# Performance work log

Hardware: AMD Instinct MI355X
Metric: run time of the kernel (lower is better)

Reference implementation:

```python
import jax, jax.numpy as jnp
import numpy as np

# ---- static frequency grid from init kwargs ----
POS_FREQS = 31
W_MIN, W_MAX = 0.1, 1.0
PATCH = 16

def _build_grid():
    g = (W_MAX / W_MIN) ** (1.0 / (POS_FREQS - 1))
    pos_w = (W_MIN * g ** np.arange(POS_FREQS)).astype(np.float32)
    Wx = np.concatenate([-pos_w[::-1], [0.0], pos_w]).astype(np.float32)  # len 63
    Wy = np.concatenate([[0.0], pos_w]).astype(np.float32)               # len 32
    pad_h = (PATCH - len(Wx) % PATCH) % PATCH  # 1 -> H=64
    pad_w = (PATCH - len(Wy) % PATCH) % PATCH  # 0 -> W=32
    U, V = np.meshgrid(Wx, Wy, indexing='ij')
    U = np.pad(U, ((0, pad_h), (0, pad_w))).astype(np.float32)
    V = np.pad(V, ((0, pad_h), (0, pad_w))).astype(np.float32)
    pad_mask = np.ones_like(U)
    if pad_h > 0:
        pad_mask[-pad_h:, :] = 0.0
    if pad_w > 0:
        pad_mask[:, -pad_w:] = 0.0
    return U, V, pad_mask

_U, _V, _PADMASK = _build_grid()
H, W = _U.shape


def _cft_triangles(tris):
    """Closed-form CFT of each triangle over the HxW frequency grid.
    tris: [T,3,2] float32 -> [T,H,W] complex64."""
    pi = np.float32(np.pi)
    U = jnp.asarray(_U)[None]  # [1,H,W]
    V = jnp.asarray(_V)[None]
    xq = tris[:, 0, 0][:, None, None]; yq = tris[:, 0, 1][:, None, None]
    xr = tris[:, 1, 0][:, None, None]; yr = tris[:, 1, 1][:, None, None]
    xs = tris[:, 2, 0][:, None, None]; ys = tris[:, 2, 1][:, None, None]
    det = xq * (yr - ys) + xr * (ys - yq) + xs * (yq - yr)
    area = jnp.abs(0.5 * det)  # [T,1,1]
    U_ = U * (xr - xq) + V * (yr - yq)  # [T,H,W]
    V_ = U * (xs - xr) + V * (ys - yr)
    phase_shift = jnp.exp(-2j * pi * (U * xq + V * yq))
    zero_mask = (U_ == 0) & (V_ == 0)
    diag_mask = (U_ + V_ == 0) & ~zero_mask
    u_mask = (U_ == 0) & ~zero_mask
    v_mask = (V_ == 0) & ~zero_mask
    normal_mask = ~(diag_mask | zero_mask | u_mask | v_mask)
    four_pi2 = np.float32(4.0) * pi * pi

    def inv_safe(den, m):
        # masked reciprocal with safe denominator (keeps grads finite)
        return jnp.where(m, 1.0, 0.0) / jnp.where(m, den, 1.0)

    part1 = (inv_safe(four_pi2 * U_ * V_ * (U_ + V_), normal_mask)
             - inv_safe(four_pi2 * U_ * U_, diag_mask)
             - inv_safe(four_pi2 * V_ * V_, u_mask)
             + inv_safe(four_pi2 * U_ * U_, v_mask))
    base_u = jnp.exp(-2j * pi * U_)
    base_v = jnp.exp(-2j * pi * V_)
    base_uv = jnp.exp(-2j * pi * (U_ + V_))
    j2pi = 2j * pi
    part2 = (jnp.where(normal_mask, -U_ * base_uv + (U_ + V_) * base_u - V_, 0.0)
             + jnp.where(diag_mask, base_u + j2pi * U_ - 1.0, 0.0)
             + jnp.where(u_mask, base_v + j2pi * V_ - 1.0, 0.0)
             + jnp.where(v_mask, (j2pi * U_ + 1.0) * base_u - 1.0, 0.0))
    FT = 2.0 * area * part1 * part2 * phase_shift
    FT = jnp.where(zero_mask, area.astype(jnp.complex64), FT)
    return FT * jnp.asarray(_PADMASK)[None]


def _forward(batch_triangles, lengths):
    B, maxN = batch_triangles.shape[:2]
    FT = _cft_triangles(batch_triangles.reshape(B * maxN, 3, 2))
    FT = FT.reshape(B, maxN, H, W)
    valid = (jnp.arange(maxN)[None, :] < lengths[:, None]).astype(jnp.float32)
    FT_total = jnp.sum(FT * valid[:, :, None, None], axis=1)  # segment-sum by polygon
    re, im = FT_total.real, FT_total.imag
    m2 = re * re + im * im
    is0 = m2 == 0
    mag = jnp.where(is0, 0.0, jnp.sqrt(jnp.where(is0, 1.0, m2)))
    phase = jnp.arctan2(im, jnp.where(is0, 1.0, re))  # angle(0)=0 like torch
    mag = jnp.log1p(mag)
    return mag[:, None], phase[:, None]  # [B,1,H,W] each


def setup_inputs() -> dict:
    key = jax.random.key(0)
    k1, k2 = jax.random.split(key)
    batch_triangles = jax.random.normal(k1, (64, 128, 3, 2), dtype=jnp.float32)
    lengths = jax.random.randint(k2, (64,), 0, 128, dtype=jnp.int32)
    return {"batch_triangles": batch_triangles, "lengths": lengths}


def reference(batch_triangles, lengths):
    return _forward(batch_triangles, lengths)
```

## Files before the change

kernel.cpp:

```cpp
#include <hip/hip_runtime.h>
#include <cmath>

#define BB     64
#define MAXN   128
#define HH     64
#define WW     32
#define NFREQ  (HH*WW)
#define BLK    256
#define NWAVE  4
#define PGRPS  (NFREQ/64)

__device__ __constant__ float c_posw[31] = {
    0.10000000000f, 0.10797751623f, 0.11659144012f, 0.12589254118f,
    0.13593563909f, 0.14677992676f, 0.15848931925f, 0.17113283042f,
    0.18478497970f, 0.19952623150f, 0.21544346900f, 0.23263050672f,
    0.25118864315f, 0.27122725793f, 0.29286445646f, 0.31622776602f,
    0.34145488738f, 0.36869450645f, 0.39810717055f, 0.42986623483f,
    0.46415888336f, 0.50118723363f, 0.54116952655f, 0.58434141336f,
    0.63095734448f, 0.68129206906f, 0.73564225446f, 0.79432823472f,
    0.85769589859f, 0.92611872813f, 1.00000000000f
};

__device__ __forceinline__ void sincos_2pi(float x, float* s, float* c) {
    float r = __builtin_amdgcn_fractf(x);
    *s = __builtin_amdgcn_sinf(r);
    *c = __builtin_amdgcn_cosf(r);
}

__device__ __forceinline__ void eval_tri(
    float U, float V, float4 A4, float4 B4, float& accR, float& accI,
    float TWOPI, float FOUR_PI2)
{
    const float xq = A4.x,  yq = A4.y,  e1x = A4.z, e1y = A4.w;
    const float e2x = B4.x, e2y = B4.y, area = B4.z;

    const float U_ = __fadd_rn(__fmul_rn(U, e1x), __fmul_rn(V, e1y));
    const float V_ = __fadd_rn(__fmul_rn(U, e2x), __fmul_rn(V, e2y));
    const float S  = __fadd_rn(U_, V_);

    const bool uz   = (U_ == 0.0f);
    const bool vz   = (V_ == 0.0f);
    const bool sz   = (S  == 0.0f);
    const bool zero = uz && vz;
    const bool diag = sz && !zero;
    const bool u_m  = uz && !zero;
    const bool v_m  = vz && !zero;
    const bool nrm  = !(uz || vz || sz);

    const float t_q = U * xq + V * yq;
    const float t_r = t_q + U_;
    const float t_s = t_r + V_;

    float s_q, c_q, s_r, c_r, s_s, c_s;
    sincos_2pi(t_q, &s_q, &c_q);
    sincos_2pi(t_r, &s_r, &c_r);
    sincos_2pi(t_s, &s_s, &c_s);

    const float twU = TWOPI * U_;
    const float twV = TWOPI * V_;

    const float Ac = nrm ? -U_ : (u_m ? 1.0f : 0.0f);
    const float Bc = nrm ?  S  : ((diag || v_m) ? 1.0f : 0.0f);
    const float Cc = nrm ? -V_ : -1.0f;
    const float Dc = v_m  ? twU : 0.0f;
    const float Ec = diag ? twU : (u_m ? twV : 0.0f);

    const float d1  = u_m ? V_ : U_;
    const float den = nrm ? (U_ * V_) * S : d1 * d1;
    const float p1  = __builtin_amdgcn_rcpf(FOUR_PI2 * den);
    const float sgn = (diag || u_m) ? -2.0f : 2.0f;
    const float k   = zero ? 0.0f : sgn * area * p1;

    const float re =  Ac * c_s + Bc * c_r + Cc * c_q + Dc * s_r + Ec * s_q;
    const float im = -(Ac * s_s + Bc * s_r + Cc * s_q) + Dc * c_r + Ec * c_q;

    accR = fmaf(k, re, accR) + (zero ? area : 0.0f);
    accI = fmaf(k, im, accI);
}

__global__ __launch_bounds__(BLK) void poly_cft_fused(
    const float* __restrict__ tris,
    const int*   __restrict__ lengths,
    float*       __restrict__ out)
{
    __shared__ float2 s_red[NWAVE][64];

    const int pg   = blockIdx.x;
    const int b    = blockIdx.y;
    const int lane = threadIdx.x & 63;
    const int wv   = threadIdx.x >> 6;
    const int p    = (pg << 6) | lane;
    const int h    = p >> 5;
    const int w    = p & 31;

    float U;
    if (h < 31)       U = -c_posw[30 - h];
    else if (h == 31) U = 0.0f;
    else if (h < 63)  U = c_posw[h - 32];
    else              U = 0.0f;
    const float V = (w == 0) ? 0.0f : c_posw[w - 1];

    const float PI_F     = 3.14159274101257324f;
    const float TWOPI    = 6.28318548202514648f;
    const float FOUR_PI2 = (4.0f * PI_F) * PI_F;

    const int N = lengths[b];
    const float* __restrict__ tb = tris + (size_t)b * MAXN * 6;

    float accR = 0.0f, accI = 0.0f;

    int n = wv;
    float xq = 0.0f, yq = 0.0f, xr = 0.0f, yr = 0.0f, xs = 0.0f, ys = 0.0f;
    if (n < N) {
        const int nn = __builtin_amdgcn_readfirstlane(n);
        const float* t = tb + nn * 6;
        xq = t[0]; yq = t[1]; xr = t[2]; yr = t[3]; xs = t[4]; ys = t[5];
    }
    while (n < N) {
        const int n2 = n + NWAVE;
        float x2q = 0.0f, y2q = 0.0f, x2r = 0.0f, y2r = 0.0f, x2s = 0.0f, y2s = 0.0f;
        if (n2 < N) {
            const int nn2 = __builtin_amdgcn_readfirstlane(n2);
            const float* t2 = tb + nn2 * 6;
            x2q = t2[0]; y2q = t2[1]; x2r = t2[2]; y2r = t2[3]; x2s = t2[4]; y2s = t2[5];
        }

        const float det  = xq * (yr - ys) + xr * (ys - yq) + xs * (yq - yr);
        const float area = fabsf(0.5f * det);
        const float4 A4 = make_float4(xq, yq, xr - xq, yr - yq);
        const float4 B4 = make_float4(xs - xr, ys - yr, area, 0.0f);
        eval_tri(U, V, A4, B4, accR, accI, TWOPI, FOUR_PI2);

        n = n2;
        xq = x2q; yq = y2q; xr = x2r; yr = y2r; xs = x2s; ys = y2s;
    }

    s_red[wv][lane] = make_float2(accR, accI);
    __syncthreads();

    if (wv == 0) {
        float R = 0.0f, I = 0.0f;
#pragma unroll
        for (int k = 0; k < NWAVE; ++k) {
            const float2 v = s_red[k][lane];
            R += v.x;
            I += v.y;
        }
        R += 0.0f;
        I += 0.0f;

        if (h == 63) { R = 0.0f; I = 0.0f; }

        const float m2 = __fadd_rn(__fmul_rn(R, R), __fmul_rn(I, I));
        float mag, ph;
        if (m2 == 0.0f) {
            mag = 0.0f;
            ph  = atan2f(I, 1.0f);
        } else {
            mag = log1pf(sqrtf(m2));
            ph  = atan2f(I, R);
        }

        const int o = b * NFREQ + p;
        out[o]              = mag;
        out[BB * NFREQ + o] = ph;
    }
}

extern "C" void kernel_launch(void* const* d_in, const int* in_sizes, int n_in,
                              void* d_out, int out_size, void* d_ws, size_t ws_size,
                              hipStream_t stream) {
    const float* tris    = (const float*)d_in[0];
    const int*   lengths = (const int*)d_in[1];
    float*       out     = (float*)d_out;

    poly_cft_fused<<<dim3(PGRPS, BB), dim3(BLK), 0, stream>>>(tris, lengths, out);
}
```

Before: 80.94 us.

## Stage triangle setup in LDS and add wave-uniform fast path for generic frequencies

Each block now precomputes per-triangle edge vectors and doubled area once into shared memory, instead of every wave reloading vertices from global memory and recomputing the determinant per iteration. The inner loop uses a ballot to take a compact branch when no lane hits a degenerate case (U_, V_ or their sum equal to zero). That branch drops the mask/select logic and uses a simplified coefficient formula. This adds a block-wide barrier and LDS traffic, and the fast path must match the general formula numerically.

```diff
diff --git a/kernel.cpp b/kernel.cpp
--- a/kernel.cpp
+++ b/kernel.cpp
@@ -27,62 +27,13 @@
     *c = __builtin_amdgcn_cosf(r);
 }
 
-__device__ __forceinline__ void eval_tri(
-    float U, float V, float4 A4, float4 B4, float& accR, float& accI,
-    float TWOPI, float FOUR_PI2)
-{
-    const float xq = A4.x,  yq = A4.y,  e1x = A4.z, e1y = A4.w;
-    const float e2x = B4.x, e2y = B4.y, area = B4.z;
-
-    const float U_ = __fadd_rn(__fmul_rn(U, e1x), __fmul_rn(V, e1y));
-    const float V_ = __fadd_rn(__fmul_rn(U, e2x), __fmul_rn(V, e2y));
-    const float S  = __fadd_rn(U_, V_);
-
-    const bool uz   = (U_ == 0.0f);
-    const bool vz   = (V_ == 0.0f);
-    const bool sz   = (S  == 0.0f);
-    const bool zero = uz && vz;
-    const bool diag = sz && !zero;
-    const bool u_m  = uz && !zero;
-    const bool v_m  = vz && !zero;
-    const bool nrm  = !(uz || vz || sz);
-
-    const float t_q = U * xq + V * yq;
-    const float t_r = t_q + U_;
-    const float t_s = t_r + V_;
-
-    float s_q, c_q, s_r, c_r, s_s, c_s;
-    sincos_2pi(t_q, &s_q, &c_q);
-    sincos_2pi(t_r, &s_r, &c_r);
-    sincos_2pi(t_s, &s_s, &c_s);
-
-    const float twU = TWOPI * U_;
-    const float twV = TWOPI * V_;
-
-    const float Ac = nrm ? -U_ : (u_m ? 1.0f : 0.0f);
-    const float Bc = nrm ?  S  : ((diag || v_m) ? 1.0f : 0.0f);
-    const float Cc = nrm ? -V_ : -1.0f;
-    const float Dc = v_m  ? twU : 0.0f;
-    const float Ec = diag ? twU : (u_m ? twV : 0.0f);
-
-    const float d1  = u_m ? V_ : U_;
-    const float den = nrm ? (U_ * V_) * S : d1 * d1;
-    const float p1  = __builtin_amdgcn_rcpf(FOUR_PI2 * den);
-    const float sgn = (diag || u_m) ? -2.0f : 2.0f;
-    const float k   = zero ? 0.0f : sgn * area * p1;
-
-    const float re =  Ac * c_s + Bc * c_r + Cc * c_q + Dc * s_r + Ec * s_q;
-    const float im = -(Ac * s_s + Bc * s_r + Cc * s_q) + Dc * c_r + Ec * c_q;
-
-    accR = fmaf(k, re, accR) + (zero ? area : 0.0f);
-    accI = fmaf(k, im, accI);
-}
-
 __global__ __launch_bounds__(BLK) void poly_cft_fused(
     const float* __restrict__ tris,
     const int*   __restrict__ lengths,
     float*       __restrict__ out)
 {
+    __shared__ float4 sA[MAXN];
+    __shared__ float4 sB[MAXN];
     __shared__ float2 s_red[NWAVE][64];
 
     const int pg   = blockIdx.x;
@@ -92,6 +43,19 @@
     const int p    = (pg << 6) | lane;
     const int h    = p >> 5;
     const int w    = p & 31;
+
+    const int N = lengths[b];
+
+    if (threadIdx.x < MAXN) {
+        const float2* tp = (const float2*)(tris + ((size_t)b * MAXN + threadIdx.x) * 6);
+        const float2 v0 = tp[0], v1 = tp[1], v2 = tp[2];
+        const float xq = v0.x, yq = v0.y, xr = v1.x, yr = v1.y, xs = v2.x, ys = v2.y;
+        const float det  = xq * (yr - ys) + xr * (ys - yq) + xs * (yq - yr);
+        const float area = fabsf(0.5f * det);
+        sA[threadIdx.x] = make_float4(xq, yq, xr - xq, yr - yq);
+        sB[threadIdx.x] = make_float4(xs - xr, ys - yr, 2.0f * area, 0.0f);
+    }
+    __syncthreads();
 
     float U;
     if (h < 31)       U = -c_posw[30 - h];
@@ -104,35 +68,65 @@
     const float TWOPI    = 6.28318548202514648f;
     const float FOUR_PI2 = (4.0f * PI_F) * PI_F;
 
-    const int N = lengths[b];
-    const float* __restrict__ tb = tris + (size_t)b * MAXN * 6;
-
     float accR = 0.0f, accI = 0.0f;
 
-    int n = wv;
-    float xq = 0.0f, yq = 0.0f, xr = 0.0f, yr = 0.0f, xs = 0.0f, ys = 0.0f;
-    if (n < N) {
-        const int nn = __builtin_amdgcn_readfirstlane(n);
-        const float* t = tb + nn * 6;
-        xq = t[0]; yq = t[1]; xr = t[2]; yr = t[3]; xs = t[4]; ys = t[5];
-    }
-    while (n < N) {
-        const int n2 = n + NWAVE;
-        float x2q = 0.0f, y2q = 0.0f, x2r = 0.0f, y2r = 0.0f, x2s = 0.0f, y2s = 0.0f;
-        if (n2 < N) {
-            const int nn2 = __builtin_amdgcn_readfirstlane(n2);
-            const float* t2 = tb + nn2 * 6;
-            x2q = t2[0]; y2q = t2[1]; x2r = t2[2]; y2r = t2[3]; x2s = t2[4]; y2s = t2[5];
+    for (int n = wv; n < N; n += NWAVE) {
+        const float4 A4 = sA[n];
+        const float4 B4 = sB[n];
+
+        const float U_ = __fadd_rn(__fmul_rn(U, A4.z), __fmul_rn(V, A4.w));
+        const float V_ = __fadd_rn(__fmul_rn(U, B4.x), __fmul_rn(V, B4.y));
+        const float S  = __fadd_rn(U_, V_);
+
+        const bool uz = (U_ == 0.0f);
+        const bool vz = (V_ == 0.0f);
+        const bool sz = (S  == 0.0f);
+
+        const float t_q = U * A4.x + V * A4.y;
+        const float t_r = t_q + U_;
+        const float t_s = t_r + V_;
+
+        float s_q, c_q, s_r, c_r, s_s, c_s;
+        sincos_2pi(t_q, &s_q, &c_q);
+        sincos_2pi(t_r, &s_r, &c_r);
+        sincos_2pi(t_s, &s_s, &c_s);
+
+        if (__ballot(uz || vz || sz)) {
+            const float area = 0.5f * B4.z;
+            const bool zero = uz && vz;
+            const bool diag = sz && !zero;
+            const bool u_m  = uz && !zero;
+            const bool v_m  = vz && !zero;
+            const bool nrm  = !(uz || vz || sz);
+
+            const float twU = TWOPI * U_;
+            const float twV = TWOPI * V_;
+
+            const float Ac = nrm ? -U_ : (u_m ? 1.0f : 0.0f);
+            const float Bc = nrm ?  S  : ((diag || v_m) ? 1.0f : 0.0f);
+            const float Cc = nrm ? -V_ : -1.0f;
+            const float Dc = v_m  ? twU : 0.0f;
+            const float Ec = diag ? twU : (u_m ? twV : 0.0f);
+
+            const float d1  = u_m ? V_ : U_;
+            const float den = nrm ? (U_ * V_) * S : d1 * d1;
+            const float p1  = __builtin_amdgcn_rcpf(FOUR_PI2 * den);
+            const float sgn = (diag || u_m) ? -2.0f : 2.0f;
+            const float k   = zero ? 0.0f : sgn * area * p1;
+
+            const float re =  Ac * c_s + Bc * c_r + Cc * c_q + Dc * s_r + Ec * s_q;
+            const float im = -(Ac * s_s + Bc * s_r + Cc * s_q) + Dc * c_r + Ec * c_q;
+
+            accR = fmaf(k, re, accR) + (zero ? area : 0.0f);
+            accI = fmaf(k, im, accI);
+        } else {
+            const float p1 = __builtin_amdgcn_rcpf(FOUR_PI2 * ((U_ * V_) * S));
+            const float k  = B4.z * p1;
+            const float re = S * c_r - U_ * c_s - V_ * c_q;
+            const float im = U_ * s_s - S * s_r + V_ * s_q;
+            accR = fmaf(k, re, accR);
+            accI = fmaf(k, im, accI);
         }
-
-        const float det  = xq * (yr - ys) + xr * (ys - yq) + xs * (yq - yr);
-        const float area = fabsf(0.5f * det);
-        const float4 A4 = make_float4(xq, yq, xr - xq, yr - yq);
-        const float4 B4 = make_float4(xs - xr, ys - yr, area, 0.0f);
-        eval_tri(U, V, A4, B4, accR, accI, TWOPI, FOUR_PI2);
-
-        n = n2;
-        xq = x2q; yq = y2q; xr = x2r; yr = y2r; xs = x2s; ys = y2s;
     }
 
     s_red[wv][lane] = make_float2(accR, accI);
```

Result: faster. 75.60 us (-6.6%).
